# Kernel tuning notes

Hardware: AMD Instinct MI355X
Metric: run time of the kernel (lower is better)

Reference implementation:

```python
import jax, jax.numpy as jnp
import numpy as np

TEMPERATURE = 0.07
SCALE_BY_TEMPERATURE = True
N = 4096
D = 256
N_POS = 32768
CHUNK = 128  # row-chunk size for the cdist to bound the [CHUNK, N, D] temp


def setup_inputs() -> dict:
    key = jax.random.key(0)
    k1, k2, k3 = jax.random.split(key, 3)
    out = jax.random.normal(k1, (N, D), dtype=jnp.float32)
    row = jax.random.randint(k2, (N_POS,), 0, N, dtype=jnp.int32)
    col = jax.random.randint(k3, (N_POS,), 0, N, dtype=jnp.int32)
    return {"out": out, "row": row, "col": col}


def _l1_cdist(x):
    """Pairwise Manhattan distance [N, N], computed in row chunks so the
    [CHUNK, N, D] broadcast temporary stays bounded."""
    n, d = x.shape
    xr = x.reshape(n // CHUNK, CHUNK, d)

    def chunk_dist(xc):  # xc: [CHUNK, D] -> [CHUNK, N]
        return jnp.sum(jnp.abs(xc[:, None, :] - x[None, :, :]), axis=-1)

    return jax.lax.map(chunk_dist, xr).reshape(n, n)


def reference(out, row, col):
    n = out.shape[0]
    sim = -_l1_cdist(out) / TEMPERATURE                      # [N, N]
    logits_max = jax.lax.stop_gradient(jnp.max(sim, axis=1, keepdims=True))
    sim = sim - logits_max
    logits_mask = 1.0 - jnp.eye(n, dtype=sim.dtype)          # zero out self-sims
    denom = jnp.log(jnp.sum(jnp.exp(sim) * logits_mask, axis=1, keepdims=True))
    log_probs = sim - denom                                  # [N, N]
    loss = -jnp.mean(log_probs[row, col])                    # gather positive pairs
    if SCALE_BY_TEMPERATURE:
        loss = loss * TEMPERATURE
    return loss
```

## Files before the change

kernel.cpp:

```cpp
#include <hip/hip_runtime.h>
#include <math.h>

#define N 4096
#define D 256
#define NPOS 32768
#define TEMP 0.07f
#define INVT (1.0f / 0.07f)
#define BIGF 3.0e38f

#define RQ 5.5f
#define QS (255.0f / (2.0f * RQ))
#define DEQ (2.0f * RQ / 255.0f)

#define NT 64
#define NT2 32
#define NTRI2 (NT2 * (NT2 + 1) / 2)
#define KC 32

#define WS_PMIN 0
#define WS_PSUM (N * NT)
#define WS_T    (2 * N * NT)
#define WS_ACC  (2 * N * NT + N)
#define WS_CNT  (2 * N * NT + N + 1)
#define WS_XQ   (2 * N * NT + N + 4)

__device__ __forceinline__ unsigned sad_u8(unsigned a, unsigned b, unsigned c) {
#if __has_builtin(__builtin_amdgcn_sad_u8)
    return __builtin_amdgcn_sad_u8(a, b, c);
#else
    unsigned d;
    asm("v_sad_u8 %0, %1, %2, %3" : "=v"(d) : "v"(a), "v"(b), "v"(c));
    return d;
#endif
}

__device__ __forceinline__ unsigned quant1(float v) {
    const float f = fminf(fmaxf((v + RQ) * QS, 0.0f), 255.0f);
    return (unsigned)__float2uint_rn(f);
}

__global__ __launch_bounds__(256)
void cvt_init_k(const float* __restrict__ x, unsigned* __restrict__ xq,
                float* __restrict__ acc, unsigned* __restrict__ cnt) {
    const int i = blockIdx.x * 256 + threadIdx.x;
    const float4 v = ((const float4*)x)[i];
    const unsigned q = quant1(v.x) | (quant1(v.y) << 8) |
                       (quant1(v.z) << 16) | (quant1(v.w) << 24);
    xq[i] = q;
    if (i == 0) { *acc = 0.0f; *cnt = 0u; }
}

__global__ __launch_bounds__(256, 3)
void dist_tile_k(const unsigned* __restrict__ xq,
                 float* __restrict__ pmin, float* __restrict__ psum) {
    const int tt = blockIdx.x;
    const int u = (NTRI2 - 1) - tt;
    int r = (int)((sqrtf((float)(8 * u + 1)) - 1.0f) * 0.5f);
    while (r * (r + 1) / 2 > u) --r;
    while ((r + 1) * (r + 2) / 2 <= u) ++r;
    const int bm = (NT2 - 1) - r;
    const int bn = (NT2 - 1) - (u - r * (r + 1) / 2);

    const int tid = threadIdx.x;
    const int lane = tid & 63;
    const int w = tid >> 6;
    const int w0 = w >> 1;
    const int w1 = w & 1;
    const int tx = lane & 7;
    const int ty = lane >> 3;

    const int rt = 2 * bm + w0;
    const int ct = 2 * bn + w1;
    const bool diagq = (rt == ct);

    __shared__ unsigned As[KC][128];
    __shared__ unsigned Bs[KC][128];

    unsigned uacc[2][2][4][4];
#pragma unroll
    for (int rh = 0; rh < 2; ++rh)
#pragma unroll
        for (int ch = 0; ch < 2; ++ch)
#pragma unroll
            for (int i = 0; i < 4; ++i)
#pragma unroll
                for (int j = 0; j < 4; ++j) uacc[rh][ch][i][j] = 0u;

    const int rowA0 = bm * 128;
    const int rowB0 = bn * 128;

    const int srow = (w < 2 ? rowA0 : rowB0) + (w & 1) * 64 + lane;
    const uint4* grow = (const uint4*)(xq + (size_t)srow * (D / 4));
    unsigned (*S)[128] = (w < 2) ? As : Bs;
    const int m = (w & 1) * 64 + lane;

    const int aoff = w0 * 64;
    const int boff = w1 * 64;

    for (int chk = 0; chk < 2; ++chk) {
        uint4 L[8];
#pragma unroll
        for (int c = 0; c < 8; ++c) L[c] = grow[chk * 8 + c];
        __syncthreads();
#pragma unroll
        for (int c = 0; c < 8; ++c) {
            S[c * 4 + 0][m] = L[c].x; S[c * 4 + 1][m] = L[c].y;
            S[c * 4 + 2][m] = L[c].z; S[c * 4 + 3][m] = L[c].w;
        }
        __syncthreads();

#pragma unroll 8
        for (int k4 = 0; k4 < KC; ++k4) {
            const uint4 alo = *(const uint4*)&As[k4][aoff + ty * 4];
            const uint4 ahi = *(const uint4*)&As[k4][aoff + 32 + ty * 4];
            const uint4 blo = *(const uint4*)&Bs[k4][boff + tx * 4];
            const uint4 bhi = *(const uint4*)&Bs[k4][boff + 32 + tx * 4];
            const unsigned av[2][4] = {{alo.x, alo.y, alo.z, alo.w},
                                       {ahi.x, ahi.y, ahi.z, ahi.w}};
            const unsigned bv[2][4] = {{blo.x, blo.y, blo.z, blo.w},
                                       {bhi.x, bhi.y, bhi.z, bhi.w}};
#pragma unroll
            for (int rh = 0; rh < 2; ++rh)
#pragma unroll
                for (int chq = 0; chq < 2; ++chq)
#pragma unroll
                    for (int i = 0; i < 4; ++i)
#pragma unroll
                        for (int j = 0; j < 4; ++j)
                            uacc[rh][chq][i][j] =
                                sad_u8(av[rh][i], bv[chq][j], uacc[rh][chq][i][j]);
        }
    }

    float acc[2][2][4][4];
#pragma unroll
    for (int rh = 0; rh < 2; ++rh)
#pragma unroll
        for (int chq = 0; chq < 2; ++chq)
#pragma unroll
            for (int i = 0; i < 4; ++i)
#pragma unroll
                for (int j = 0; j < 4; ++j)
                    acc[rh][chq][i][j] = (float)uacc[rh][chq][i][j] * DEQ;

    if (diagq) {
#pragma unroll
        for (int rh = 0; rh < 2; ++rh)
#pragma unroll
            for (int chq = 0; chq < 2; ++chq)
#pragma unroll
                for (int i = 0; i < 4; ++i)
#pragma unroll
                    for (int j = 0; j < 4; ++j)
                        if (rh * 32 + ty * 4 + i == chq * 32 + tx * 4 + j)
                            acc[rh][chq][i][j] = BIGF;
    }

    if (rt <= ct) {
#pragma unroll
        for (int rh = 0; rh < 2; ++rh) {
#pragma unroll
            for (int i = 0; i < 4; ++i) {
                float mn = BIGF;
#pragma unroll
                for (int chq = 0; chq < 2; ++chq)
#pragma unroll
                    for (int j = 0; j < 4; ++j) mn = fminf(mn, acc[rh][chq][i][j]);
                mn = fminf(mn, __shfl_xor(mn, 1, 64));
                mn = fminf(mn, __shfl_xor(mn, 2, 64));
                mn = fminf(mn, __shfl_xor(mn, 4, 64));
                float s = 0.0f;
#pragma unroll
                for (int chq = 0; chq < 2; ++chq)
#pragma unroll
                    for (int j = 0; j < 4; ++j)
                        s += __expf((mn - acc[rh][chq][i][j]) * INVT);
                s += __shfl_xor(s, 1, 64);
                s += __shfl_xor(s, 2, 64);
                s += __shfl_xor(s, 4, 64);
                if (tx == 0) {
                    const size_t idx =
                        (size_t)(rt * 64 + rh * 32 + ty * 4 + i) * NT + ct;
                    pmin[idx] = mn;
                    psum[idx] = s;
                }
            }
        }
    }

    if (rt < ct) {
#pragma unroll
        for (int chq = 0; chq < 2; ++chq) {
#pragma unroll
            for (int j = 0; j < 4; ++j) {
                float mn = BIGF;
#pragma unroll
                for (int rh = 0; rh < 2; ++rh)
#pragma unroll
                    for (int i = 0; i < 4; ++i) mn = fminf(mn, acc[rh][chq][i][j]);
                mn = fminf(mn, __shfl_xor(mn, 8, 64));
                mn = fminf(mn, __shfl_xor(mn, 16, 64));
                mn = fminf(mn, __shfl_xor(mn, 32, 64));
                float s = 0.0f;
#pragma unroll
                for (int rh = 0; rh < 2; ++rh)
#pragma unroll
                    for (int i = 0; i < 4; ++i)
                        s += __expf((mn - acc[rh][chq][i][j]) * INVT);
                s += __shfl_xor(s, 8, 64);
                s += __shfl_xor(s, 16, 64);
                s += __shfl_xor(s, 32, 64);
                if (ty == 0) {
                    const size_t idx =
                        (size_t)(ct * 64 + chq * 32 + tx * 4 + j) * NT + rt;
                    pmin[idx] = mn;
                    psum[idx] = s;
                }
            }
        }
    }
}

__global__ __launch_bounds__(256)
void row_stats_k(const float* __restrict__ pmin, const float* __restrict__ psum,
                 float* __restrict__ t) {
    const int r = blockIdx.x * 4 + (threadIdx.x >> 6);
    const int c = threadIdx.x & 63;
    const float pm = pmin[(size_t)r * NT + c];
    const float ps = psum[(size_t)r * NT + c];
    float mn = pm;
#pragma unroll
    for (int off = 32; off > 0; off >>= 1) mn = fminf(mn, __shfl_xor(mn, off, 64));
    float s = ps * __expf((mn - pm) * INVT);
#pragma unroll
    for (int off = 32; off > 0; off >>= 1) s += __shfl_xor(s, off, 64);
    if (c == 0) t[r] = TEMP * __logf(s) - mn;
}

__global__ __launch_bounds__(256)
void pair_fin_k(const float* __restrict__ x, const int* __restrict__ row,
                const int* __restrict__ col, const float* __restrict__ t,
                float* __restrict__ acc, unsigned* __restrict__ cnt,
                float* __restrict__ out) {
    const int lane = threadIdx.x & 63;
    const int wave = threadIdx.x >> 6;
    const int p0 = (blockIdx.x * 4 + wave) * 8;

    int rp[8], cp[8];
#pragma unroll
    for (int i = 0; i < 8; ++i) { rp[i] = row[p0 + i]; cp[i] = col[p0 + i]; }
    float4 a[8], b[8];
#pragma unroll
    for (int i = 0; i < 8; ++i) {
        a[i] = *(const float4*)&x[(size_t)rp[i] * D + lane * 4];
        b[i] = *(const float4*)&x[(size_t)cp[i] * D + lane * 4];
    }
    float wsum = 0.0f;
#pragma unroll
    for (int i = 0; i < 8; ++i) {
        float d = fabsf(a[i].x - b[i].x) + fabsf(a[i].y - b[i].y) +
                  fabsf(a[i].z - b[i].z) + fabsf(a[i].w - b[i].w);
#pragma unroll
        for (int off = 32; off > 0; off >>= 1) d += __shfl_xor(d, off, 64);
        if (lane == 0) wsum += d + t[rp[i]];
    }

    __shared__ float bs[4];
    if (lane == 0) bs[wave] = wsum;
    __syncthreads();
    if (threadIdx.x == 0) {
        const float tot = bs[0] + bs[1] + bs[2] + bs[3];
        atomicAdd(acc, tot);
        __threadfence();
        const unsigned tk = atomicAdd(cnt, 1u);
        if (tk == (unsigned)(gridDim.x - 1)) {
            const float v = atomicAdd(acc, 0.0f);
            out[0] = v * (1.0f / (float)NPOS);
        }
    }
}

extern "C" void kernel_launch(void* const* d_in, const int* in_sizes, int n_in,
                              void* d_out, int out_size, void* d_ws, size_t ws_size,
                              hipStream_t stream) {
    const float* x = (const float*)d_in[0];
    const int* row = (const int*)d_in[1];
    const int* col = (const int*)d_in[2];
    float* ws = (float*)d_ws;
    float* out = (float*)d_out;
    unsigned* xq = (unsigned*)(ws + WS_XQ);
    float* acc = ws + WS_ACC;
    unsigned* cnt = (unsigned*)(ws + WS_CNT);

    cvt_init_k<<<(N * D / 4) / 256, 256, 0, stream>>>(x, xq, acc, cnt);

    dist_tile_k<<<NTRI2, 256, 0, stream>>>(xq, ws + WS_PMIN, ws + WS_PSUM);

    row_stats_k<<<N / 4, 256, 0, stream>>>(ws + WS_PMIN, ws + WS_PSUM, ws + WS_T);

    pair_fin_k<<<NPOS / 32, 256, 0, stream>>>(x, row, col, ws + WS_T, acc, cnt, out);
}
```

Measured before the change: 133.2 us.

## Pad LDS tiles, coalesce global loads, and double-buffer LDS reads in SAD loop

Changes the L1-distance tile kernel's staging: each thread now loads 16-byte chunks spread across rows so global reads coalesce better, and the shared tiles are padded to 132 columns to avoid bank conflicts on the transposed stores. The inner loop prefetches the next k-slice from LDS into registers while running the current SAD accumulations, and uses inline asm v_sad_u8 with an in-place accumulator. Launch bounds are lowered to 2 waves-per-SIMD hint, which allows more registers for the prefetch at the cost of occupancy.

```diff
diff --git a/kernel.cpp b/kernel.cpp
--- a/kernel.cpp
+++ b/kernel.cpp
@@ -16,6 +16,7 @@
 #define NT2 32
 #define NTRI2 (NT2 * (NT2 + 1) / 2)
 #define KC 32
+#define LP 132
 
 #define WS_PMIN 0
 #define WS_PSUM (N * NT)
@@ -24,14 +25,8 @@
 #define WS_CNT  (2 * N * NT + N + 1)
 #define WS_XQ   (2 * N * NT + N + 4)
 
-__device__ __forceinline__ unsigned sad_u8(unsigned a, unsigned b, unsigned c) {
-#if __has_builtin(__builtin_amdgcn_sad_u8)
-    return __builtin_amdgcn_sad_u8(a, b, c);
-#else
-    unsigned d;
-    asm("v_sad_u8 %0, %1, %2, %3" : "=v"(d) : "v"(a), "v"(b), "v"(c));
-    return d;
-#endif
+__device__ __forceinline__ void sad_acc(unsigned a, unsigned b, unsigned& c) {
+    asm("v_sad_u8 %0, %1, %2, %0" : "+v"(c) : "v"(a), "v"(b));
 }
 
 __device__ __forceinline__ unsigned quant1(float v) {
@@ -50,16 +45,16 @@
     if (i == 0) { *acc = 0.0f; *cnt = 0u; }
 }
 
-__global__ __launch_bounds__(256, 3)
+__global__ __launch_bounds__(256, 2)
 void dist_tile_k(const unsigned* __restrict__ xq,
                  float* __restrict__ pmin, float* __restrict__ psum) {
     const int tt = blockIdx.x;
-    const int u = (NTRI2 - 1) - tt;
-    int r = (int)((sqrtf((float)(8 * u + 1)) - 1.0f) * 0.5f);
-    while (r * (r + 1) / 2 > u) --r;
-    while ((r + 1) * (r + 2) / 2 <= u) ++r;
+    const int u_ = (NTRI2 - 1) - tt;
+    int r = (int)((sqrtf((float)(8 * u_ + 1)) - 1.0f) * 0.5f);
+    while (r * (r + 1) / 2 > u_) --r;
+    while ((r + 1) * (r + 2) / 2 <= u_) ++r;
     const int bm = (NT2 - 1) - r;
-    const int bn = (NT2 - 1) - (u - r * (r + 1) / 2);
+    const int bn = (NT2 - 1) - (u_ - r * (r + 1) / 2);
 
     const int tid = threadIdx.x;
     const int lane = tid & 63;
@@ -73,8 +68,8 @@
     const int ct = 2 * bn + w1;
     const bool diagq = (rt == ct);
 
-    __shared__ unsigned As[KC][128];
-    __shared__ unsigned Bs[KC][128];
+    __shared__ unsigned As[KC][LP];
+    __shared__ unsigned Bs[KC][LP];
 
     unsigned uacc[2][2][4][4];
 #pragma unroll
@@ -89,32 +84,59 @@
     const int rowA0 = bm * 128;
     const int rowB0 = bn * 128;
 
-    const int srow = (w < 2 ? rowA0 : rowB0) + (w & 1) * 64 + lane;
-    const uint4* grow = (const uint4*)(xq + (size_t)srow * (D / 4));
-    unsigned (*S)[128] = (w < 2) ? As : Bs;
-    const int m = (w & 1) * 64 + lane;
-
-    const int aoff = w0 * 64;
-    const int boff = w1 * 64;
+    const int su = tid & 3;
+    const int ra = tid >> 2;
+    const uint4* gA0 = (const uint4*)xq + (size_t)(rowA0 + ra) * 16;
+    const uint4* gA1 = (const uint4*)xq + (size_t)(rowA0 + ra + 64) * 16;
+    const uint4* gB0 = (const uint4*)xq + (size_t)(rowB0 + ra) * 16;
+    const uint4* gB1 = (const uint4*)xq + (size_t)(rowB0 + ra + 64) * 16;
+
+    const int aoff = w0 * 64 + ty * 4;
+    const int boff = w1 * 64 + tx * 4;
 
     for (int chk = 0; chk < 2; ++chk) {
-        uint4 L[8];
-#pragma unroll
-        for (int c = 0; c < 8; ++c) L[c] = grow[chk * 8 + c];
+        const int cb = chk * 8;
+        const uint4 a00 = gA0[cb + su];
+        const uint4 a01 = gA0[cb + su + 4];
+        const uint4 a10 = gA1[cb + su];
+        const uint4 a11 = gA1[cb + su + 4];
+        const uint4 b00 = gB0[cb + su];
+        const uint4 b01 = gB0[cb + su + 4];
+        const uint4 b10 = gB1[cb + su];
+        const uint4 b11 = gB1[cb + su + 4];
         __syncthreads();
-#pragma unroll
-        for (int c = 0; c < 8; ++c) {
-            S[c * 4 + 0][m] = L[c].x; S[c * 4 + 1][m] = L[c].y;
-            S[c * 4 + 2][m] = L[c].z; S[c * 4 + 3][m] = L[c].w;
+        {
+            const int k0 = su * 4, k1 = (su + 4) * 4;
+            As[k0 + 0][ra] = a00.x; As[k0 + 1][ra] = a00.y;
+            As[k0 + 2][ra] = a00.z; As[k0 + 3][ra] = a00.w;
+            As[k1 + 0][ra] = a01.x; As[k1 + 1][ra] = a01.y;
+            As[k1 + 2][ra] = a01.z; As[k1 + 3][ra] = a01.w;
+            As[k0 + 0][ra + 64] = a10.x; As[k0 + 1][ra + 64] = a10.y;
+            As[k0 + 2][ra + 64] = a10.z; As[k0 + 3][ra + 64] = a10.w;
+            As[k1 + 0][ra + 64] = a11.x; As[k1 + 1][ra + 64] = a11.y;
+            As[k1 + 2][ra + 64] = a11.z; As[k1 + 3][ra + 64] = a11.w;
+            Bs[k0 + 0][ra] = b00.x; Bs[k0 + 1][ra] = b00.y;
+            Bs[k0 + 2][ra] = b00.z; Bs[k0 + 3][ra] = b00.w;
+            Bs[k1 + 0][ra] = b01.x; Bs[k1 + 1][ra] = b01.y;
+            Bs[k1 + 2][ra] = b01.z; Bs[k1 + 3][ra] = b01.w;
+            Bs[k0 + 0][ra + 64] = b10.x; Bs[k0 + 1][ra + 64] = b10.y;
+            Bs[k0 + 2][ra + 64] = b10.z; Bs[k0 + 3][ra + 64] = b10.w;
+            Bs[k1 + 0][ra + 64] = b11.x; Bs[k1 + 1][ra + 64] = b11.y;
+            Bs[k1 + 2][ra + 64] = b11.z; Bs[k1 + 3][ra + 64] = b11.w;
         }
         __syncthreads();
 
-#pragma unroll 8
+        uint4 alo = *(const uint4*)&As[0][aoff];
+        uint4 ahi = *(const uint4*)&As[0][aoff + 32];
+        uint4 blo = *(const uint4*)&Bs[0][boff];
+        uint4 bhi = *(const uint4*)&Bs[0][boff + 32];
+#pragma unroll 4
         for (int k4 = 0; k4 < KC; ++k4) {
-            const uint4 alo = *(const uint4*)&As[k4][aoff + ty * 4];
-            const uint4 ahi = *(const uint4*)&As[k4][aoff + 32 + ty * 4];
-            const uint4 blo = *(const uint4*)&Bs[k4][boff + tx * 4];
-            const uint4 bhi = *(const uint4*)&Bs[k4][boff + 32 + tx * 4];
+            const int kn = (k4 + 1) & (KC - 1);
+            const uint4 nal = *(const uint4*)&As[kn][aoff];
+            const uint4 nah = *(const uint4*)&As[kn][aoff + 32];
+            const uint4 nbl = *(const uint4*)&Bs[kn][boff];
+            const uint4 nbh = *(const uint4*)&Bs[kn][boff + 32];
             const unsigned av[2][4] = {{alo.x, alo.y, alo.z, alo.w},
                                        {ahi.x, ahi.y, ahi.z, ahi.w}};
             const unsigned bv[2][4] = {{blo.x, blo.y, blo.z, blo.w},
@@ -127,8 +149,8 @@
                     for (int i = 0; i < 4; ++i)
 #pragma unroll
                         for (int j = 0; j < 4; ++j)
-                            uacc[rh][chq][i][j] =
-                                sad_u8(av[rh][i], bv[chq][j], uacc[rh][chq][i][j]);
+                            sad_acc(av[rh][i], bv[chq][j], uacc[rh][chq][i][j]);
+            alo = nal; ahi = nah; blo = nbl; bhi = nbh;
         }
     }
 
```

Measured after the change: 133.5 us. Within noise of the previous version (+0.2%).

## Use single-wave 64x64 triangular tiles instead of 4-wave 128x128 blocks

Applied to the files above, without the earlier changes.

Reworks the distance kernel so each block is a single 64-thread wavefront computing one 64x64 upper-triangular tile, giving 2080 blocks instead of 528 four-wave blocks. Shared tiles shrink to 64 rows with a padded leading dimension of 68 to reduce bank conflicts, and the global load pattern becomes row-strided and coalesced across lanes. The intent is better load balance and less synchronization cost within a block, with in-place SAD accumulation. The trade-off is less reuse of loaded data per block and more global traffic, since the total number of tile loads roughly doubles.

```diff
diff --git a/kernel.cpp b/kernel.cpp
--- a/kernel.cpp
+++ b/kernel.cpp
@@ -13,9 +13,9 @@
 #define DEQ (2.0f * RQ / 255.0f)
 
 #define NT 64
-#define NT2 32
-#define NTRI2 (NT2 * (NT2 + 1) / 2)
+#define NTRI (NT * (NT + 1) / 2)
 #define KC 32
+#define LP 68
 
 #define WS_PMIN 0
 #define WS_PSUM (N * NT)
@@ -24,13 +24,11 @@
 #define WS_CNT  (2 * N * NT + N + 1)
 #define WS_XQ   (2 * N * NT + N + 4)
 
-__device__ __forceinline__ unsigned sad_u8(unsigned a, unsigned b, unsigned c) {
+__device__ __forceinline__ void sad_acc(unsigned a, unsigned b, unsigned& c) {
 #if __has_builtin(__builtin_amdgcn_sad_u8)
-    return __builtin_amdgcn_sad_u8(a, b, c);
+    c = __builtin_amdgcn_sad_u8(a, b, c);
 #else
-    unsigned d;
-    asm("v_sad_u8 %0, %1, %2, %3" : "=v"(d) : "v"(a), "v"(b), "v"(c));
-    return d;
+    asm("v_sad_u8 %0, %1, %2, %0" : "+v"(c) : "v"(a), "v"(b));
 #endif
 }
 
@@ -50,31 +48,24 @@
     if (i == 0) { *acc = 0.0f; *cnt = 0u; }
 }
 
-__global__ __launch_bounds__(256, 3)
+__global__ __launch_bounds__(64, 2)
 void dist_tile_k(const unsigned* __restrict__ xq,
                  float* __restrict__ pmin, float* __restrict__ psum) {
     const int tt = blockIdx.x;
-    const int u = (NTRI2 - 1) - tt;
-    int r = (int)((sqrtf((float)(8 * u + 1)) - 1.0f) * 0.5f);
-    while (r * (r + 1) / 2 > u) --r;
-    while ((r + 1) * (r + 2) / 2 <= u) ++r;
-    const int bm = (NT2 - 1) - r;
-    const int bn = (NT2 - 1) - (u - r * (r + 1) / 2);
-
-    const int tid = threadIdx.x;
-    const int lane = tid & 63;
-    const int w = tid >> 6;
-    const int w0 = w >> 1;
-    const int w1 = w & 1;
+    const int u_ = (NTRI - 1) - tt;
+    int r = (int)((sqrtf((float)(8 * u_ + 1)) - 1.0f) * 0.5f);
+    while (r * (r + 1) / 2 > u_) --r;
+    while ((r + 1) * (r + 2) / 2 <= u_) ++r;
+    const int bm = (NT - 1) - r;
+    const int bn = (NT - 1) - (u_ - r * (r + 1) / 2);
+    const bool diag = (bm == bn);
+
+    const int lane = threadIdx.x;
     const int tx = lane & 7;
     const int ty = lane >> 3;
 
-    const int rt = 2 * bm + w0;
-    const int ct = 2 * bn + w1;
-    const bool diagq = (rt == ct);
-
-    __shared__ unsigned As[KC][128];
-    __shared__ unsigned Bs[KC][128];
+    __shared__ unsigned As[KC][LP];
+    __shared__ unsigned Bs[KC][LP];
 
     unsigned uacc[2][2][4][4];
 #pragma unroll
@@ -86,35 +77,41 @@
 #pragma unroll
                 for (int j = 0; j < 4; ++j) uacc[rh][ch][i][j] = 0u;
 
-    const int rowA0 = bm * 128;
-    const int rowB0 = bn * 128;
-
-    const int srow = (w < 2 ? rowA0 : rowB0) + (w & 1) * 64 + lane;
-    const uint4* grow = (const uint4*)(xq + (size_t)srow * (D / 4));
-    unsigned (*S)[128] = (w < 2) ? As : Bs;
-    const int m = (w & 1) * 64 + lane;
-
-    const int aoff = w0 * 64;
-    const int boff = w1 * 64;
+    const int rowA0 = bm * 64;
+    const int rowB0 = bn * 64;
+
+    const int su = lane & 7;
+    const int r0 = lane >> 3;
+    const uint4* gA = (const uint4*)xq + (size_t)(rowA0 + r0) * 16 + su;
+    const uint4* gB = (const uint4*)xq + (size_t)(rowB0 + r0) * 16 + su;
+
+    const int aoff = ty * 4;
+    const int boff = tx * 4;
 
     for (int chk = 0; chk < 2; ++chk) {
-        uint4 L[8];
-#pragma unroll
-        for (int c = 0; c < 8; ++c) L[c] = grow[chk * 8 + c];
+        const int gbase = chk * 8;
+        uint4 la[8], lb[8];
+#pragma unroll
+        for (int c = 0; c < 8; ++c) la[c] = gA[gbase + (size_t)c * 128];
+#pragma unroll
+        for (int c = 0; c < 8; ++c) lb[c] = gB[gbase + (size_t)c * 128];
         __syncthreads();
 #pragma unroll
         for (int c = 0; c < 8; ++c) {
-            S[c * 4 + 0][m] = L[c].x; S[c * 4 + 1][m] = L[c].y;
-            S[c * 4 + 2][m] = L[c].z; S[c * 4 + 3][m] = L[c].w;
+            const int rr = r0 + 8 * c;
+            As[su * 4 + 0][rr] = la[c].x; As[su * 4 + 1][rr] = la[c].y;
+            As[su * 4 + 2][rr] = la[c].z; As[su * 4 + 3][rr] = la[c].w;
+            Bs[su * 4 + 0][rr] = lb[c].x; Bs[su * 4 + 1][rr] = lb[c].y;
+            Bs[su * 4 + 2][rr] = lb[c].z; Bs[su * 4 + 3][rr] = lb[c].w;
         }
         __syncthreads();
 
 #pragma unroll 8
         for (int k4 = 0; k4 < KC; ++k4) {
-            const uint4 alo = *(const uint4*)&As[k4][aoff + ty * 4];
-            const uint4 ahi = *(const uint4*)&As[k4][aoff + 32 + ty * 4];
-            const uint4 blo = *(const uint4*)&Bs[k4][boff + tx * 4];
-            const uint4 bhi = *(const uint4*)&Bs[k4][boff + 32 + tx * 4];
+            const uint4 alo = *(const uint4*)&As[k4][aoff];
+            const uint4 ahi = *(const uint4*)&As[k4][aoff + 32];
+            const uint4 blo = *(const uint4*)&Bs[k4][boff];
+            const uint4 bhi = *(const uint4*)&Bs[k4][boff + 32];
             const unsigned av[2][4] = {{alo.x, alo.y, alo.z, alo.w},
                                        {ahi.x, ahi.y, ahi.z, ahi.w}};
             const unsigned bv[2][4] = {{blo.x, blo.y, blo.z, blo.w},
@@ -127,8 +124,7 @@
                     for (int i = 0; i < 4; ++i)
 #pragma unroll
                         for (int j = 0; j < 4; ++j)
-                            uacc[rh][chq][i][j] =
-                                sad_u8(av[rh][i], bv[chq][j], uacc[rh][chq][i][j]);
+                            sad_acc(av[rh][i], bv[chq][j], uacc[rh][chq][i][j]);
         }
     }
 
@@ -143,7 +139,7 @@
                 for (int j = 0; j < 4; ++j)
                     acc[rh][chq][i][j] = (float)uacc[rh][chq][i][j] * DEQ;
 
-    if (diagq) {
+    if (diag) {
 #pragma unroll
         for (int rh = 0; rh < 2; ++rh)
 #pragma unroll
@@ -156,7 +152,7 @@
                             acc[rh][chq][i][j] = BIGF;
     }
 
-    if (rt <= ct) {
+    {
 #pragma unroll
         for (int rh = 0; rh < 2; ++rh) {
 #pragma unroll
@@ -180,7 +176,7 @@
                 s += __shfl_xor(s, 4, 64);
                 if (tx == 0) {
                     const size_t idx =
-                        (size_t)(rt * 64 + rh * 32 + ty * 4 + i) * NT + ct;
+                        (size_t)(rowA0 + rh * 32 + ty * 4 + i) * NT + bn;
                     pmin[idx] = mn;
                     psum[idx] = s;
                 }
@@ -188,7 +184,7 @@
         }
     }
 
-    if (rt < ct) {
+    if (!diag) {
 #pragma unroll
         for (int chq = 0; chq < 2; ++chq) {
 #pragma unroll
@@ -212,7 +208,7 @@
                 s += __shfl_xor(s, 32, 64);
                 if (ty == 0) {
                     const size_t idx =
-                        (size_t)(ct * 64 + chq * 32 + tx * 4 + j) * NT + rt;
+                        (size_t)(rowB0 + chq * 32 + tx * 4 + j) * NT + bm;
                     pmin[idx] = mn;
                     psum[idx] = s;
                 }
@@ -294,7 +290,7 @@
 
     cvt_init_k<<<(N * D / 4) / 256, 256, 0, stream>>>(x, xq, acc, cnt);
 
-    dist_tile_k<<<NTRI2, 256, 0, stream>>>(xq, ws + WS_PMIN, ws + WS_PSUM);
+    dist_tile_k<<<NTRI, 64, 0, stream>>>(xq, ws + WS_PMIN, ws + WS_PSUM);
 
     row_stats_k<<<N / 4, 256, 0, stream>>>(ws + WS_PMIN, ws + WS_PSUM, ws + WS_T);
 
```

Measured after the change: 134.3 us. About the same (+0.8%).
